# Performance work log

Hardware: AMD Instinct MI355X
Metric: run time of the kernel (lower is better)

Reference implementation:

```python
import jax, jax.numpy as jnp
import numpy as np

SIGMA = 0.1
GAMMA = 1.0 / (SIGMA * SIGMA)  # keops-style gauss kernel: exp(-|x-y|^2 / sigma^2)
B, N, D = 1, 8192, 3


def setup_inputs() -> dict:
    key = jax.random.key(0)
    k1, k2 = jax.random.split(key)
    control_points = jax.random.uniform(k1, (B, N, D), dtype=jnp.float32)
    mom = jax.random.normal(k2, (B, N, D), dtype=jnp.float32) * 0.1
    return {"mom": mom, "control_points": control_points}


def _pairwise_dist2(x, y):
    # x:[B,N,D], y:[B,M,D] -> [B,N,M] squared distances (no N x M x D intermediate)
    x2 = jnp.sum(x * x, -1)  # [B,N]
    y2 = jnp.sum(y * y, -1)  # [B,M]
    xy = jnp.einsum('bnd,bmd->bnm', x, y)
    return x2[:, :, None] + y2[:, None, :] - 2.0 * xy


def gauss_kernel(x, y, b):
    # K(x,y) b : [B,N,d]
    K = jnp.exp(-GAMMA * _pairwise_dist2(x, y))  # [B,N,M]
    return jnp.einsum('bnm,bmd->bnd', K, b)


def gauss_grad_kernel(p, x):
    # dH/dx_i = sum_j d/dx_i[exp(-g|x_i-x_j|^2)] <p_i,p_j>
    #         = -2g * sum_j K_ij <p_i,p_j> (x_i - x_j)
    K = jnp.exp(-GAMMA * _pairwise_dist2(x, x))        # [B,N,N]
    W = K * jnp.einsum('bnd,bmd->bnm', p, p)           # [B,N,N] weighted by <p_i,p_j>
    row_sum = jnp.sum(W, -1)                           # [B,N]
    Wx = jnp.einsum('bnm,bmd->bnd', W, x)              # [B,N,D]
    return (-2.0 * GAMMA) * (x * row_sum[:, :, None] - Wx)


def reference(mom, control_points):
    # variational_evolve: (dp/dt, dx/dt)
    dmom = -gauss_grad_kernel(mom, control_points)
    dx = gauss_kernel(control_points, control_points, mom)
    return (dmom, dx)
```

## Files before the change

### kernel.cpp

```cpp
#include <hip/hip_runtime.h>


#define TPB 256
#define ITILE 2
constexpr float GAMMA_C = 100.0f;
constexpr float LOG2E_C = 1.4426950408889634f;
constexpr float SB_C    = 2.0f * GAMMA_C * LOG2E_C;
constexpr float SC_C    = -GAMMA_C * LOG2E_C;
constexpr float LN2_C   = 0.69314718055994531f;

__global__ __launch_bounds__(TPB, 4) void lddmm_partial(
    const float* __restrict__ mom, const float* __restrict__ xpt,
    float* __restrict__ part, int N, int SEG, int JT) {
  extern __shared__ float4 smem[];
  float4* sA = smem;
  float4* sP = smem + JT;
  const int tid = threadIdx.x;
  const int seg = blockIdx.y;

  for (int t = tid; t < JT; t += TPB) {
    const int j = seg * JT + t;
    const float bx = xpt[3*j], by = xpt[3*j+1], bz = xpt[3*j+2];
    sA[t] = make_float4(SB_C*bx, SB_C*by, SB_C*bz,
                        SC_C * fmaf(bx, bx, fmaf(by, by, bz*bz)));
    sP[t] = make_float4(mom[3*j], mom[3*j+1], mom[3*j+2], 0.f);
  }
  __syncthreads();

  const int i0 = blockIdx.x * (TPB * ITILE) + tid;
  const int i1 = i0 + TPB;

  const float x0 = xpt[3*i0], y0 = xpt[3*i0+1], z0 = xpt[3*i0+2];
  const float p0x = mom[3*i0], p0y = mom[3*i0+1], p0z = mom[3*i0+2];
  const float c0 = SC_C * fmaf(x0, x0, fmaf(y0, y0, z0*z0));
  const float x1 = xpt[3*i1], y1 = xpt[3*i1+1], z1 = xpt[3*i1+2];
  const float p1x = mom[3*i1], p1y = mom[3*i1+1], p1z = mom[3*i1+2];
  const float c1 = SC_C * fmaf(x1, x1, fmaf(y1, y1, z1*z1));

  float wx0=0.f, wy0=0.f, wz0=0.f, gx0=0.f, gy0=0.f, gz0=0.f;
  float wx1=0.f, wy1=0.f, wz1=0.f, gx1=0.f, gy1=0.f, gz1=0.f;

#pragma unroll 4
  for (int t = 0; t < JT; ++t) {
    const float4 A = sA[t];
    const float4 P = sP[t];
    {
      const float arg = fmaf(A.x, x0, fmaf(A.y, y0, fmaf(A.z, z0, c0 + A.w)));
      const float K   = __builtin_amdgcn_exp2f(arg);
      const float dot = fmaf(P.x, p0x, fmaf(P.y, p0y, P.z * p0z));
      const float w   = K * dot;
      wx0 = fmaf(w, A.x, wx0); wy0 = fmaf(w, A.y, wy0); wz0 = fmaf(w, A.z, wz0);
      gx0 = fmaf(K, P.x, gx0); gy0 = fmaf(K, P.y, gy0); gz0 = fmaf(K, P.z, gz0);
    }
    {
      const float arg = fmaf(A.x, x1, fmaf(A.y, y1, fmaf(A.z, z1, c1 + A.w)));
      const float K   = __builtin_amdgcn_exp2f(arg);
      const float dot = fmaf(P.x, p1x, fmaf(P.y, p1y, P.z * p1z));
      const float w   = K * dot;
      wx1 = fmaf(w, A.x, wx1); wy1 = fmaf(w, A.y, wy1); wz1 = fmaf(w, A.z, wz1);
      gx1 = fmaf(K, P.x, gx1); gy1 = fmaf(K, P.y, gy1); gz1 = fmaf(K, P.z, gz1);
    }
  }

  const size_t SN = (size_t)SEG * N;
  float* p = part + (size_t)seg * N;
  p[0*SN+i0] = wx0; p[0*SN+i1] = wx1;
  p[1*SN+i0] = wy0; p[1*SN+i1] = wy1;
  p[2*SN+i0] = wz0; p[2*SN+i1] = wz1;
  p[3*SN+i0] = gx0; p[3*SN+i1] = gx1;
  p[4*SN+i0] = gy0; p[4*SN+i1] = gy1;
  p[5*SN+i0] = gz0; p[5*SN+i1] = gz1;
}

__global__ __launch_bounds__(TPB) void lddmm_reduce(
    const float* __restrict__ part, float* __restrict__ R, int N, int SEG) {
  const int i = blockIdx.x * TPB + threadIdx.x;
  const int c = blockIdx.y;
  const float* src = part + (size_t)c * SEG * N + i;
  float s0 = 0.f, s1 = 0.f, s2 = 0.f, s3 = 0.f;
  int s = 0;
  for (; s + 4 <= SEG; s += 4) {
    s0 += src[(size_t)(s+0)*N]; s1 += src[(size_t)(s+1)*N];
    s2 += src[(size_t)(s+2)*N]; s3 += src[(size_t)(s+3)*N];
  }
  for (; s < SEG; ++s) s0 += src[(size_t)s*N];
  R[(size_t)c * N + i] = (s0 + s1) + (s2 + s3);
}

__global__ __launch_bounds__(TPB) void lddmm_finalize(
    const float* __restrict__ R, const float* __restrict__ xpt,
    const float* __restrict__ mom, float* __restrict__ out, int N) {
  const int i = blockIdx.x * TPB + threadIdx.x;
  const float WX = R[(size_t)0*N+i], WY = R[(size_t)1*N+i], WZ = R[(size_t)2*N+i];
  const float GX = R[(size_t)3*N+i], GY = R[(size_t)4*N+i], GZ = R[(size_t)5*N+i];
  const float xi = xpt[3*i], yi = xpt[3*i+1], zi = xpt[3*i+2];
  const float px = mom[3*i], py = mom[3*i+1], pz = mom[3*i+2];
  const float A  = fmaf(px, GX, fmaf(py, GY, pz * GZ));
  const float TGA = 2.0f * GAMMA_C * A;
  out[3*i+0] = fmaf(TGA, xi, -LN2_C * WX);
  out[3*i+1] = fmaf(TGA, yi, -LN2_C * WY);
  out[3*i+2] = fmaf(TGA, zi, -LN2_C * WZ);
  out[3*N + 3*i + 0] = GX;
  out[3*N + 3*i + 1] = GY;
  out[3*N + 3*i + 2] = GZ;
}

__global__ __launch_bounds__(TPB) void lddmm_atomic(
    const float* __restrict__ mom, const float* __restrict__ xpt,
    float* __restrict__ out, int N) {
  const int i  = blockIdx.x * TPB + threadIdx.x;
  const int jb = blockIdx.y * TPB;
  __shared__ float4 sA[TPB], sP[TPB];
  {
    const int j = jb + threadIdx.x;
    const float bx = xpt[3*j], by = xpt[3*j+1], bz = xpt[3*j+2];
    sA[threadIdx.x] = make_float4(SB_C*bx, SB_C*by, SB_C*bz,
                                  SC_C * fmaf(bx, bx, fmaf(by, by, bz*bz)));
    sP[threadIdx.x] = make_float4(mom[3*j], mom[3*j+1], mom[3*j+2], 0.f);
  }
  __syncthreads();
  const float xi = xpt[3*i], yi = xpt[3*i+1], zi = xpt[3*i+2];
  const float pxi = mom[3*i], pyi = mom[3*i+1], pzi = mom[3*i+2];
  const float ci = SC_C * fmaf(xi, xi, fmaf(yi, yi, zi*zi));
  float a=0.f, wx=0.f, wy=0.f, wz=0.f, gx=0.f, gy=0.f, gz=0.f;
#pragma unroll 4
  for (int t = 0; t < TPB; ++t) {
    const float4 A = sA[t], P = sP[t];
    const float arg = fmaf(A.x, xi, fmaf(A.y, yi, fmaf(A.z, zi, ci + A.w)));
    const float K   = __builtin_amdgcn_exp2f(arg);
    const float dot = fmaf(P.x, pxi, fmaf(P.y, pyi, P.z * pzi));
    const float w   = K * dot;
    a += w;
    wx = fmaf(w, A.x, wx); wy = fmaf(w, A.y, wy); wz = fmaf(w, A.z, wz);
    gx = fmaf(K, P.x, gx); gy = fmaf(K, P.y, gy); gz = fmaf(K, P.z, gz);
  }
  const float TGA = 2.0f * GAMMA_C * a;
  atomicAdd(&out[3*i+0], fmaf(TGA, xi, -LN2_C * wx));
  atomicAdd(&out[3*i+1], fmaf(TGA, yi, -LN2_C * wy));
  atomicAdd(&out[3*i+2], fmaf(TGA, zi, -LN2_C * wz));
  atomicAdd(&out[3*N+3*i+0], gx);
  atomicAdd(&out[3*N+3*i+1], gy);
  atomicAdd(&out[3*N+3*i+2], gz);
}

extern "C" void kernel_launch(void* const* d_in, const int* in_sizes, int n_in,
                              void* d_out, int out_size, void* d_ws, size_t ws_size,
                              hipStream_t stream) {
  const float* mom = (const float*)d_in[0];
  const float* xpt = (const float*)d_in[1];
  float* out = (float*)d_out;
  const int N = in_sizes[0] / 3;

  auto need = [&](int s) { return (size_t)(6*s + 6) * (size_t)N * sizeof(float); };
  int SEG = 64;
  while (SEG > 2 && need(SEG) > ws_size) SEG >>= 1;

  const bool shapes_ok = (N % (TPB * ITILE) == 0) && (N % SEG == 0) &&
                         (N % TPB == 0) && ((N / SEG) <= TPB);
  if (need(SEG) <= ws_size && shapes_ok) {
    const int JT = N / SEG;
    float* partb = (float*)d_ws;
    float* R     = partb + (size_t)6 * SEG * N;
    const size_t shmem = (size_t)JT * 2 * sizeof(float4);
    dim3 gA(N / (TPB * ITILE), SEG);
    lddmm_partial<<<gA, TPB, shmem, stream>>>(mom, xpt, partb, N, SEG, JT);
    dim3 gB(N / TPB, 6);
    lddmm_reduce<<<gB, TPB, 0, stream>>>(partb, R, N, SEG);
    lddmm_finalize<<<N / TPB, TPB, 0, stream>>>(R, xpt, mom, out, N);
  } else {
    hipMemsetAsync(d_out, 0, (size_t)out_size * sizeof(float), stream);
    dim3 grid(N / TPB, N / TPB);
    lddmm_atomic<<<grid, TPB, 0, stream>>>(mom, xpt, out, N);
  }
}
```

Before: 94.94 us.

## Fuse partial, reduce and finalize into one cooperative kernel with grid sync

Replaces the three-kernel sequence (partial sums, segment reduction, finalize) with a single cooperative launch. A grid-wide barrier separates the pairwise accumulation from the reduction, and the reduction assigns 8 lanes per point, with shuffles gathering the six components for finalize. This removes two launch gaps and the intermediate R buffer round trip. In exchange it needs the whole grid (16x64 blocks) to be co-resident and adds the cost of a grid barrier; the old three-kernel path is kept as a fallback if the cooperative launch fails.

```diff
diff --git a/kernel.cpp b/kernel.cpp
--- a/kernel.cpp
+++ b/kernel.cpp
@@ -1,4 +1,7 @@
 #include <hip/hip_runtime.h>
+#include <hip/hip_cooperative_groups.h>
+
+namespace cg = cooperative_groups;
 
 
 #define TPB 256
@@ -8,6 +11,112 @@
 constexpr float SB_C    = 2.0f * GAMMA_C * LOG2E_C;
 constexpr float SC_C    = -GAMMA_C * LOG2E_C;
 constexpr float LN2_C   = 0.69314718055994531f;
+
+__global__ __launch_bounds__(TPB, 4) void lddmm_fused(
+    const float* __restrict__ mom, const float* __restrict__ xpt,
+    float* __restrict__ part, float* __restrict__ out,
+    int N, int SEG, int JT) {
+  extern __shared__ float4 smem[];
+  float4* sA = smem;
+  float4* sP = smem + JT;
+  const int tid = threadIdx.x;
+  const int seg = blockIdx.y;
+
+  for (int t = tid; t < JT; t += TPB) {
+    const int j = seg * JT + t;
+    const float bx = xpt[3*j], by = xpt[3*j+1], bz = xpt[3*j+2];
+    sA[t] = make_float4(SB_C*bx, SB_C*by, SB_C*bz,
+                        SC_C * fmaf(bx, bx, fmaf(by, by, bz*bz)));
+    sP[t] = make_float4(mom[3*j], mom[3*j+1], mom[3*j+2], 0.f);
+  }
+  __syncthreads();
+
+  const int i0 = blockIdx.x * (TPB * ITILE) + tid;
+  const int i1 = i0 + TPB;
+
+  const float x0 = xpt[3*i0], y0 = xpt[3*i0+1], z0 = xpt[3*i0+2];
+  const float p0x = mom[3*i0], p0y = mom[3*i0+1], p0z = mom[3*i0+2];
+  const float c0 = SC_C * fmaf(x0, x0, fmaf(y0, y0, z0*z0));
+  const float x1 = xpt[3*i1], y1 = xpt[3*i1+1], z1 = xpt[3*i1+2];
+  const float p1x = mom[3*i1], p1y = mom[3*i1+1], p1z = mom[3*i1+2];
+  const float c1 = SC_C * fmaf(x1, x1, fmaf(y1, y1, z1*z1));
+
+  float wx0=0.f, wy0=0.f, wz0=0.f, gx0=0.f, gy0=0.f, gz0=0.f;
+  float wx1=0.f, wy1=0.f, wz1=0.f, gx1=0.f, gy1=0.f, gz1=0.f;
+
+#pragma unroll 4
+  for (int t = 0; t < JT; ++t) {
+    const float4 A = sA[t];
+    const float4 P = sP[t];
+    {
+      const float arg = fmaf(A.x, x0, fmaf(A.y, y0, fmaf(A.z, z0, c0 + A.w)));
+      const float K   = __builtin_amdgcn_exp2f(arg);
+      const float dot = fmaf(P.x, p0x, fmaf(P.y, p0y, P.z * p0z));
+      const float w   = K * dot;
+      wx0 = fmaf(w, A.x, wx0); wy0 = fmaf(w, A.y, wy0); wz0 = fmaf(w, A.z, wz0);
+      gx0 = fmaf(K, P.x, gx0); gy0 = fmaf(K, P.y, gy0); gz0 = fmaf(K, P.z, gz0);
+    }
+    {
+      const float arg = fmaf(A.x, x1, fmaf(A.y, y1, fmaf(A.z, z1, c1 + A.w)));
+      const float K   = __builtin_amdgcn_exp2f(arg);
+      const float dot = fmaf(P.x, p1x, fmaf(P.y, p1y, P.z * p1z));
+      const float w   = K * dot;
+      wx1 = fmaf(w, A.x, wx1); wy1 = fmaf(w, A.y, wy1); wz1 = fmaf(w, A.z, wz1);
+      gx1 = fmaf(K, P.x, gx1); gy1 = fmaf(K, P.y, gy1); gz1 = fmaf(K, P.z, gz1);
+    }
+  }
+
+  const size_t SN = (size_t)SEG * N;
+  {
+    float* p = part + (size_t)seg * N;
+    p[0*SN+i0] = wx0; p[0*SN+i1] = wx1;
+    p[1*SN+i0] = wy0; p[1*SN+i1] = wy1;
+    p[2*SN+i0] = wz0; p[2*SN+i1] = wz1;
+    p[3*SN+i0] = gx0; p[3*SN+i1] = gx1;
+    p[4*SN+i0] = gy0; p[4*SN+i1] = gy1;
+    p[5*SN+i0] = gz0; p[5*SN+i1] = gz1;
+  }
+
+  __threadfence();
+  cg::this_grid().sync();
+
+  const int gbid = blockIdx.y * gridDim.x + blockIdx.x;
+  const int gtid = gbid * TPB + tid;
+  if (gtid >= 8 * N) return;
+
+  const int c  = gtid & 7;
+  const int i  = gtid >> 3;
+  float s = 0.f;
+  if (c < 6) {
+    const float* src = part + (size_t)c * SN + i;
+    float s0 = 0.f, s1 = 0.f, s2 = 0.f, s3 = 0.f;
+    int t = 0;
+    for (; t + 4 <= SEG; t += 4) {
+      s0 += src[(size_t)(t+0)*N]; s1 += src[(size_t)(t+1)*N];
+      s2 += src[(size_t)(t+2)*N]; s3 += src[(size_t)(t+3)*N];
+    }
+    for (; t < SEG; ++t) s0 += src[(size_t)t*N];
+    s = (s0 + s1) + (s2 + s3);
+  }
+  const int lane = tid & 63;
+  const int base = lane & ~7;
+  const float WX = __shfl(s, base+0, 64), WY = __shfl(s, base+1, 64);
+  const float WZ = __shfl(s, base+2, 64);
+  const float GX = __shfl(s, base+3, 64), GY = __shfl(s, base+4, 64);
+  const float GZ = __shfl(s, base+5, 64);
+  if (c == 0) {
+    const float xi = xpt[3*i], yi = xpt[3*i+1], zi = xpt[3*i+2];
+    const float px = mom[3*i], py = mom[3*i+1], pz = mom[3*i+2];
+    const float A  = fmaf(px, GX, fmaf(py, GY, pz * GZ));
+    const float TGA = 2.0f * GAMMA_C * A;
+    out[3*i+0] = fmaf(TGA, xi, -LN2_C * WX);
+    out[3*i+1] = fmaf(TGA, yi, -LN2_C * WY);
+    out[3*i+2] = fmaf(TGA, zi, -LN2_C * WZ);
+    out[3*N + 3*i + 0] = GX;
+    out[3*N + 3*i + 1] = GY;
+    out[3*N + 3*i + 2] = GZ;
+  }
+}
 
 __global__ __launch_bounds__(TPB, 4) void lddmm_partial(
     const float* __restrict__ mom, const float* __restrict__ xpt,
@@ -17,7 +126,6 @@
   float4* sP = smem + JT;
   const int tid = threadIdx.x;
   const int seg = blockIdx.y;
-
   for (int t = tid; t < JT; t += TPB) {
     const int j = seg * JT + t;
     const float bx = xpt[3*j], by = xpt[3*j+1], bz = xpt[3*j+2];
@@ -26,20 +134,16 @@
     sP[t] = make_float4(mom[3*j], mom[3*j+1], mom[3*j+2], 0.f);
   }
   __syncthreads();
-
   const int i0 = blockIdx.x * (TPB * ITILE) + tid;
   const int i1 = i0 + TPB;
-
   const float x0 = xpt[3*i0], y0 = xpt[3*i0+1], z0 = xpt[3*i0+2];
   const float p0x = mom[3*i0], p0y = mom[3*i0+1], p0z = mom[3*i0+2];
   const float c0 = SC_C * fmaf(x0, x0, fmaf(y0, y0, z0*z0));
   const float x1 = xpt[3*i1], y1 = xpt[3*i1+1], z1 = xpt[3*i1+2];
   const float p1x = mom[3*i1], p1y = mom[3*i1+1], p1z = mom[3*i1+2];
   const float c1 = SC_C * fmaf(x1, x1, fmaf(y1, y1, z1*z1));
-
   float wx0=0.f, wy0=0.f, wz0=0.f, gx0=0.f, gy0=0.f, gz0=0.f;
   float wx1=0.f, wy1=0.f, wz1=0.f, gx1=0.f, gy1=0.f, gz1=0.f;
-
 #pragma unroll 4
   for (int t = 0; t < JT; ++t) {
     const float4 A = sA[t];
@@ -61,7 +165,6 @@
       gx1 = fmaf(K, P.x, gx1); gy1 = fmaf(K, P.y, gy1); gz1 = fmaf(K, P.z, gz1);
     }
   }
-
   const size_t SN = (size_t)SEG * N;
   float* p = part + (size_t)seg * N;
   p[0*SN+i0] = wx0; p[0*SN+i1] = wx1;
@@ -156,17 +259,28 @@
   while (SEG > 2 && need(SEG) > ws_size) SEG >>= 1;
 
   const bool shapes_ok = (N % (TPB * ITILE) == 0) && (N % SEG == 0) &&
-                         (N % TPB == 0) && ((N / SEG) <= TPB);
+                         (N % TPB == 0) && ((8 * N) % 64 == 0) &&
+                         (SEG >= 8 * ITILE);
   if (need(SEG) <= ws_size && shapes_ok) {
-    const int JT = N / SEG;
+    int JT = N / SEG;
     float* partb = (float*)d_ws;
     float* R     = partb + (size_t)6 * SEG * N;
     const size_t shmem = (size_t)JT * 2 * sizeof(float4);
     dim3 gA(N / (TPB * ITILE), SEG);
-    lddmm_partial<<<gA, TPB, shmem, stream>>>(mom, xpt, partb, N, SEG, JT);
-    dim3 gB(N / TPB, 6);
-    lddmm_reduce<<<gB, TPB, 0, stream>>>(partb, R, N, SEG);
-    lddmm_finalize<<<N / TPB, TPB, 0, stream>>>(R, xpt, mom, out, N);
+
+    int Nv = N, SEGv = SEG, JTv = JT;
+    void* args[] = { (void*)&mom, (void*)&xpt, (void*)&partb, (void*)&out,
+                     (void*)&Nv, (void*)&SEGv, (void*)&JTv };
+    hipError_t e = hipLaunchCooperativeKernel((const void*)lddmm_fused,
+                                              gA, dim3(TPB), args,
+                                              (unsigned int)shmem, stream);
+    if (e != hipSuccess) {
+      (void)hipGetLastError();
+      lddmm_partial<<<gA, TPB, shmem, stream>>>(mom, xpt, partb, N, SEG, JT);
+      dim3 gB(N / TPB, 6);
+      lddmm_reduce<<<gB, TPB, 0, stream>>>(partb, R, N, SEG);
+      lddmm_finalize<<<N / TPB, TPB, 0, stream>>>(R, xpt, mom, out, N);
+    }
   } else {
     hipMemsetAsync(d_out, 0, (size_t)out_size * sizeof(float), stream);
     dim3 grid(N / TPB, N / TPB);
```

Result: slower. 247.8 us (+161.0%).
